# Kernel tuning notes

Hardware: AMD Instinct MI355X
Metric: run time of the kernel (lower is better)

The kernel has to match this reference:

```python
import jax, jax.numpy as jnp
import numpy as np

N_CFG, N_AST, N_PT, N_FT = 20000, 100000, 50, 10
NUM_NODES = {'cfg': N_CFG, 'ast': N_AST, 'pt': N_PT, 'ft': N_FT}
# canonical etypes as (src_type, dst_type); order matches the W/b stacks
ETYPES = [('cfg', 'cfg'), ('ast', 'ast'), ('ast', 'cfg'), ('cfg', 'ast'),
          ('pt', 'cfg'), ('cfg', 'pt'), ('ft', 'cfg'), ('cfg', 'ft')]
E_COUNTS = [80000, 300000, 100000, 100000, 100000, 100000, 40000, 40000]
H = 128
LAB_F, CON_F = 80, 300
NUM_CLASSES = 2


def hetero_gcn_layer(h, W, b, edge_src, edge_dst):
    """Per-etype linear on src feats, copy_u message, per-etype mean reduce,
    'sum' cross-etype reduce (DGL hetero-GCN pattern used by GCNLayerOld)."""
    out = {nt: 0.0 for nt in NUM_NODES}
    for i, (st, dt) in enumerate(ETYPES):
        Wh = h[st] @ W[i] + b[i]                       # [N_src, d_out]
        m = Wh[edge_src[i]]                            # [E, d_out] gather
        s = jax.ops.segment_sum(m, edge_dst[i], num_segments=NUM_NODES[dt])
        cnt = jax.ops.segment_sum(jnp.ones((m.shape[0],), m.dtype),
                                  edge_dst[i], num_segments=NUM_NODES[dt])
        out[dt] = out[dt] + s / jnp.maximum(cnt, 1.0)[:, None]
    return out


def setup_inputs():
    key = jax.random.key(0)
    ks = iter(jax.random.split(key, 64))
    inp = {}
    inp['cfg_label'] = jax.random.uniform(next(ks), (N_CFG, LAB_F), jnp.float32)
    inp['cfg_content'] = jax.random.normal(next(ks), (N_CFG, CON_F), jnp.float32)
    inp['ast_label'] = jax.random.uniform(next(ks), (N_AST, LAB_F), jnp.float32)
    inp['ast_content'] = jax.random.normal(next(ks), (N_AST, CON_F), jnp.float32)
    names = ['cfgcfg', 'astast', 'astcfg', 'cfgast', 'ptcfg', 'cfgpt', 'ftcfg', 'cfgft']
    for nm, (st, dt), ne in zip(names, ETYPES, E_COUNTS):
        inp['src_' + nm] = jax.random.randint(next(ks), (ne,), 0, NUM_NODES[st], jnp.int32)
        inp['dst_' + nm] = jax.random.randint(next(ks), (ne,), 0, NUM_NODES[dt], jnp.int32)

    def lin(k, shape):
        s = 1.0 / np.sqrt(shape[-2])
        return jax.random.uniform(k, shape, jnp.float32, -s, s)

    inp['W_cfg_lab'] = lin(next(ks), (LAB_F, H // 2)); inp['b_cfg_lab'] = 0.01 * jax.random.normal(next(ks), (H // 2,), jnp.float32)
    inp['W_cfg_con'] = lin(next(ks), (CON_F, H // 2)); inp['b_cfg_con'] = 0.01 * jax.random.normal(next(ks), (H // 2,), jnp.float32)
    inp['W_ast_lab'] = lin(next(ks), (LAB_F, H // 2)); inp['b_ast_lab'] = 0.01 * jax.random.normal(next(ks), (H // 2,), jnp.float32)
    inp['W_ast_con'] = lin(next(ks), (CON_F, H // 2)); inp['b_ast_con'] = 0.01 * jax.random.normal(next(ks), (H // 2,), jnp.float32)
    inp['ptest_emb'] = jax.random.normal(next(ks), (H,), jnp.float32)
    inp['ftest_emb'] = jax.random.normal(next(ks), (H,), jnp.float32)
    for nm, (din, dout) in zip(['1', '2', '3', '4', '5'],
                               [(H, H), (H, H), (2 * H, 2 * H), (2 * H, 2 * H), (4 * H, H)]):
        inp['W' + nm] = lin(next(ks), (8, din, dout))
        inp['b' + nm] = 0.01 * jax.random.normal(next(ks), (8, dout), jnp.float32)
    inp['W_dec'] = lin(next(ks), (H, NUM_CLASSES))
    inp['b_dec'] = 0.01 * jax.random.normal(next(ks), (NUM_CLASSES,), jnp.float32)
    return inp


def reference(cfg_label, cfg_content, ast_label, ast_content,
              src_cfgcfg, dst_cfgcfg, src_astast, dst_astast,
              src_astcfg, dst_astcfg, src_cfgast, dst_cfgast,
              src_ptcfg, dst_ptcfg, src_cfgpt, dst_cfgpt,
              src_ftcfg, dst_ftcfg, src_cfgft, dst_cfgft,
              W_cfg_lab, b_cfg_lab, W_cfg_con, b_cfg_con,
              W_ast_lab, b_ast_lab, W_ast_con, b_ast_con,
              ptest_emb, ftest_emb,
              W1, b1, W2, b2, W3, b3, W4, b4, W5, b5, W_dec, b_dec):
    edge_src = [src_cfgcfg, src_astast, src_astcfg, src_cfgast,
                src_ptcfg, src_cfgpt, src_ftcfg, src_cfgft]
    edge_dst = [dst_cfgcfg, dst_astast, dst_astcfg, dst_cfgast,
                dst_ptcfg, dst_cfgpt, dst_ftcfg, dst_cfgft]
    # per-type encoders / embedding broadcast
    h = {
        'cfg': jnp.concatenate([cfg_label @ W_cfg_lab + b_cfg_lab,
                                cfg_content @ W_cfg_con + b_cfg_con], -1),
        'ast': jnp.concatenate([ast_label @ W_ast_lab + b_ast_lab,
                                ast_content @ W_ast_con + b_ast_con], -1),
        'pt': jnp.broadcast_to(ptest_emb, (N_PT, H)),
        'ft': jnp.broadcast_to(ftest_emb, (N_FT, H)),
    }
    h = hetero_gcn_layer(h, W1, b1, edge_src, edge_dst)
    saved = h
    h = hetero_gcn_layer(h, W2, b2, edge_src, edge_dst)
    h = {nt: jnp.concatenate([saved[nt], h[nt]], -1) for nt in h}   # [*, 2H]
    h = hetero_gcn_layer(h, W3, b3, edge_src, edge_dst)
    saved = h
    h = hetero_gcn_layer(h, W4, b4, edge_src, edge_dst)
    h = {nt: jnp.concatenate([saved[nt], h[nt]], -1) for nt in h}   # [*, 4H]
    h = hetero_gcn_layer(h, W5, b5, edge_src, edge_dst)             # [*, H]
    cfg_logits = h['cfg'] @ W_dec + b_dec
    ast_logits = h['ast'] @ W_dec + b_dec
    # [2*(N_CFG+N_AST), num_classes]: cfg logits, cfg pred, ast logits, ast pred
    return jnp.concatenate([cfg_logits, jax.nn.softmax(cfg_logits, -1),
                            ast_logits, jax.nn.softmax(ast_logits, -1)], 0)
```

## Files before the change

kernel.cpp:

```cpp
#include <hip/hip_runtime.h>

#define BM 64
#define BN 64
#define BK 16

__global__ __launch_bounds__(256) void gemm_bias_kernel(
    const float* __restrict__ A, int lda,
    const float* __restrict__ W,
    const float* __restrict__ bias,
    float* __restrict__ C, int ldc, int col0,
    int N, int K, int DOUT)
{
    __shared__ float As[BK][BM + 4];
    __shared__ float Bs[BK][BN + 4];
    const int tid = threadIdx.x;
    const int tx = tid & 15, ty = tid >> 4;
    const int m0 = blockIdx.x * BM, n0 = blockIdx.y * BN;
    float acc[4][4] = {};
    const int ar = tid >> 2, ak = (tid & 3) << 2;
    const int br = tid >> 4, bn = (tid & 15) << 2;

    for (int k0 = 0; k0 < K; k0 += BK) {
        float4 av = make_float4(0.f, 0.f, 0.f, 0.f);
        int grow = m0 + ar, gk = k0 + ak;
        if (grow < N) {
            if (gk + 3 < K) {
                av = *(const float4*)(A + (long long)grow * lda + gk);
            } else {
                float t0 = 0.f, t1 = 0.f, t2 = 0.f, t3 = 0.f;
                if (gk + 0 < K) t0 = A[(long long)grow * lda + gk + 0];
                if (gk + 1 < K) t1 = A[(long long)grow * lda + gk + 1];
                if (gk + 2 < K) t2 = A[(long long)grow * lda + gk + 2];
                if (gk + 3 < K) t3 = A[(long long)grow * lda + gk + 3];
                av = make_float4(t0, t1, t2, t3);
            }
        }
        As[ak + 0][ar] = av.x; As[ak + 1][ar] = av.y;
        As[ak + 2][ar] = av.z; As[ak + 3][ar] = av.w;

        float4 bv = make_float4(0.f, 0.f, 0.f, 0.f);
        int gbk = k0 + br, gn = n0 + bn;
        if (gbk < K && gn + 3 < DOUT)
            bv = *(const float4*)(W + (long long)gbk * DOUT + gn);
        *(float4*)&Bs[br][bn] = bv;
        __syncthreads();

        #pragma unroll
        for (int kk = 0; kk < BK; ++kk) {
            float4 a4 = *(const float4*)&As[kk][ty << 2];
            float4 b4 = *(const float4*)&Bs[kk][tx << 2];
            float a[4] = {a4.x, a4.y, a4.z, a4.w};
            float b[4] = {b4.x, b4.y, b4.z, b4.w};
            #pragma unroll
            for (int i = 0; i < 4; ++i)
                #pragma unroll
                for (int j = 0; j < 4; ++j)
                    acc[i][j] = fmaf(a[i], b[j], acc[i][j]);
        }
        __syncthreads();
    }

    #pragma unroll
    for (int i = 0; i < 4; ++i) {
        int gm = m0 + (ty << 2) + i;
        if (gm >= N) continue;
        #pragma unroll
        for (int j = 0; j < 4; ++j) {
            int gn = n0 + (tx << 2) + j;
            if (gn < DOUT)
                C[(long long)gm * ldc + col0 + gn] = acc[i][j] + bias[gn];
        }
    }
}

#define GM 128
#define GN 128
#define GK 16

__global__ __launch_bounds__(256) void gemm128_kernel(
    const float* __restrict__ A, int lda,
    const float* __restrict__ W,
    const float* __restrict__ bias,
    float* __restrict__ C, int ldc, int col0,
    int N, int K, int DOUT)
{
    __shared__ float As[GK][GM + 4];
    __shared__ float Bs[GK][GN + 4];
    const int tid = threadIdx.x;
    const int tx = tid & 15, ty = tid >> 4;
    const int m0 = blockIdx.x * GM, n0 = blockIdx.y * GN;
    float acc[8][8] = {};

    const int ar = tid >> 1, ak = (tid & 1) << 3;
    const int br = tid >> 4, bn = (tid & 15) << 3;

    for (int k0 = 0; k0 < K; k0 += GK) {
        int grow = m0 + ar, gk = k0 + ak;
        float4 a0 = make_float4(0.f, 0.f, 0.f, 0.f), a1 = a0;
        if (grow < N) {
            a0 = *(const float4*)(A + (long long)grow * lda + gk);
            a1 = *(const float4*)(A + (long long)grow * lda + gk + 4);
        }
        As[ak + 0][ar] = a0.x; As[ak + 1][ar] = a0.y;
        As[ak + 2][ar] = a0.z; As[ak + 3][ar] = a0.w;
        As[ak + 4][ar] = a1.x; As[ak + 5][ar] = a1.y;
        As[ak + 6][ar] = a1.z; As[ak + 7][ar] = a1.w;

        int gbk = k0 + br, gn = n0 + bn;
        float4 b0 = *(const float4*)(W + (long long)gbk * DOUT + gn);
        float4 b1 = *(const float4*)(W + (long long)gbk * DOUT + gn + 4);
        *(float4*)&Bs[br][bn] = b0;
        *(float4*)&Bs[br][bn + 4] = b1;
        __syncthreads();

        #pragma unroll
        for (int kk = 0; kk < GK; ++kk) {
            float4 aa0 = *(const float4*)&As[kk][ty << 2];
            float4 aa1 = *(const float4*)&As[kk][64 + (ty << 2)];
            float4 bb0 = *(const float4*)&Bs[kk][tx << 2];
            float4 bb1 = *(const float4*)&Bs[kk][64 + (tx << 2)];
            float a[8] = {aa0.x, aa0.y, aa0.z, aa0.w, aa1.x, aa1.y, aa1.z, aa1.w};
            float b[8] = {bb0.x, bb0.y, bb0.z, bb0.w, bb1.x, bb1.y, bb1.z, bb1.w};
            #pragma unroll
            for (int i = 0; i < 8; ++i)
                #pragma unroll
                for (int j = 0; j < 8; ++j)
                    acc[i][j] = fmaf(a[i], b[j], acc[i][j]);
        }
        __syncthreads();
    }

    #pragma unroll
    for (int half = 0; half < 2; ++half) {
        #pragma unroll
        for (int i = 0; i < 4; ++i) {
            int gm = m0 + half * 64 + (ty << 2) + i;
            if (gm >= N) continue;
            int ai = half * 4 + i;
            #pragma unroll
            for (int jh = 0; jh < 2; ++jh) {
                int gn = n0 + jh * 64 + (tx << 2);
                float4 r;
                r.x = acc[ai][jh * 4 + 0] + bias[gn + 0];
                r.y = acc[ai][jh * 4 + 1] + bias[gn + 1];
                r.z = acc[ai][jh * 4 + 2] + bias[gn + 2];
                r.w = acc[ai][jh * 4 + 3] + bias[gn + 3];
                *(float4*)(C + (long long)gm * ldc + col0 + gn) = r;
            }
        }
    }
}

template<int DOUT, bool ACC>
__global__ __launch_bounds__(256) void agg_wave_kernel(
    const float* __restrict__ Wh,
    const int* __restrict__ roff, const int* __restrict__ csr,
    float* __restrict__ out, int ldo, int col0, int N)
{
    constexpr int CT = DOUT / 4;
    constexpr int NPB = 256 / CT;
    const int node = blockIdx.x * NPB + threadIdx.x / CT;
    if (node >= N) return;
    const int c = threadIdx.x % CT;
    const int beg = roff[node], end = roff[node + 1];
    float sx = 0.f, sy = 0.f, sz = 0.f, sw = 0.f;
    for (int e = beg; e < end; ++e) {
        const int s = csr[e];
        const float4 v = *(const float4*)(Wh + (long long)s * DOUT + (c << 2));
        sx += v.x; sy += v.y; sz += v.z; sw += v.w;
    }
    const int deg = end - beg;
    const float sc = deg > 0 ? 1.0f / (float)deg : 0.0f;
    float* po = out + (long long)node * ldo + col0 + (c << 2);
    float4 r; r.x = sx * sc; r.y = sy * sc; r.z = sz * sc; r.w = sw * sc;
    if (ACC) {
        const float4 o = *(const float4*)po;
        r.x += o.x; r.y += o.y; r.z += o.z; r.w += o.w;
    }
    *(float4*)po = r;
}

template<int DOUT>
__global__ __launch_bounds__(256) void agg_part_kernel(
    const float* __restrict__ Wh,
    const int* __restrict__ roff, const int* __restrict__ csr,
    float* __restrict__ P, int SEGS)
{
    constexpr int CT = DOUT / 4;
    constexpr int EP = 256 / CT;
    const int node = blockIdx.x / SEGS;
    const int seg  = blockIdx.x % SEGS;
    const int c = threadIdx.x % CT;
    const int g = threadIdx.x / CT;
    const int beg = roff[node], end = roff[node + 1];
    float sx = 0.f, sy = 0.f, sz = 0.f, sw = 0.f;
    for (int e = beg + seg * EP + g; e < end; e += SEGS * EP) {
        const int s = csr[e];
        const float4 v = *(const float4*)(Wh + (long long)s * DOUT + (c << 2));
        sx += v.x; sy += v.y; sz += v.z; sw += v.w;
    }
    __shared__ float4 red[256];
    red[threadIdx.x] = make_float4(sx, sy, sz, sw);
    __syncthreads();
    if (g == 0) {
        #pragma unroll
        for (int k = 1; k < EP; ++k) {
            const float4 v = red[k * CT + c];
            sx += v.x; sy += v.y; sz += v.z; sw += v.w;
        }
        float* pp = P + (long long)node * DOUT + (c << 2);
        atomicAdd(pp + 0, sx);
        atomicAdd(pp + 1, sy);
        atomicAdd(pp + 2, sz);
        atomicAdd(pp + 3, sw);
    }
}

__global__ void agg_fin_kernel(const float* __restrict__ P,
                               const int* __restrict__ roff,
                               float* __restrict__ out, int ldo, int col0,
                               int N, int DOUT)
{
    int idx = blockIdx.x * blockDim.x + threadIdx.x;
    if (idx >= N * DOUT) return;
    int n = idx / DOUT, c = idx % DOUT;
    int deg = roff[n + 1] - roff[n];
    float sc = deg > 0 ? 1.0f / (float)deg : 0.0f;
    out[(long long)n * ldo + col0 + c] = P[idx] * sc;
}

__global__ void zero_f32_kernel(float* __restrict__ p, int n)
{
    int i = blockIdx.x * blockDim.x + threadIdx.x;
    if (i < n) p[i] = 0.f;
}

__global__ void zero_i32_kernel(int* __restrict__ p, int n)
{
    int i = blockIdx.x * blockDim.x + threadIdx.x;
    if (i < n) p[i] = 0;
}

__global__ void count_kernel(const int* __restrict__ dst, int E, int* __restrict__ cnt)
{
    int i = blockIdx.x * blockDim.x + threadIdx.x;
    if (i < E) atomicAdd(&cnt[dst[i]], 1);
}

struct ScanParams { int off[8]; int N[8]; };

__global__ __launch_bounds__(1024) void scan8_kernel(
    const int* __restrict__ cnt_all, int* __restrict__ roff_all, ScanParams p)
{
    const int et = blockIdx.x;
    const int* cnt = cnt_all + p.off[et];
    int* roff = roff_all + p.off[et] + et;
    const int N = p.N[et];
    __shared__ int sh[1024];
    __shared__ int carry_sh;
    if (threadIdx.x == 0) carry_sh = 0;
    __syncthreads();
    for (int base = 0; base < N; base += 1024) {
        const int i = base + threadIdx.x;
        const int v = (i < N) ? cnt[i] : 0;
        sh[threadIdx.x] = v;
        __syncthreads();
        int incl = v;
        for (int ofs = 1; ofs < 1024; ofs <<= 1) {
            const int t = (threadIdx.x >= (unsigned)ofs) ? sh[threadIdx.x - ofs] : 0;
            __syncthreads();
            incl += t;
            sh[threadIdx.x] = incl;
            __syncthreads();
        }
        const int carry = carry_sh;
        if (i < N) roff[i] = carry + incl - v;
        __syncthreads();
        if (threadIdx.x == 1023) carry_sh = carry + incl;
        __syncthreads();
    }
    if (threadIdx.x == 0) roff[N] = carry_sh;
}

__global__ void fill_kernel(const int* __restrict__ src, const int* __restrict__ dst,
                            int E, const int* __restrict__ roff,
                            int* __restrict__ cur, int* __restrict__ csr)
{
    int i = blockIdx.x * blockDim.x + threadIdx.x;
    if (i < E) {
        const int d = dst[i];
        const int pos = atomicAdd(&cur[d], 1);
        csr[roff[d] + pos] = src[i];
    }
}

__global__ void bcast_kernel(const float* __restrict__ emb, float* __restrict__ Fp,
                             int ld, int N)
{
    int idx = blockIdx.x * blockDim.x + threadIdx.x;
    if (idx >= N * 128) return;
    int r = idx >> 7, c = idx & 127;
    Fp[(long long)r * ld + c] = emb[c];
}

__global__ void decoder_kernel(const float* __restrict__ H, int ld, int N,
                               const float* __restrict__ Wd,
                               const float* __restrict__ bd,
                               float* __restrict__ logits, float* __restrict__ soft)
{
    int n = blockIdx.x * blockDim.x + threadIdx.x;
    if (n >= N) return;
    const float* h = H + (long long)n * ld;
    float s0 = bd[0], s1 = bd[1];
    #pragma unroll
    for (int k = 0; k < 128; k += 4) {
        float4 hv = *(const float4*)(h + k);
        s0 = fmaf(hv.x, Wd[2 * (k + 0) + 0], s0); s1 = fmaf(hv.x, Wd[2 * (k + 0) + 1], s1);
        s0 = fmaf(hv.y, Wd[2 * (k + 1) + 0], s0); s1 = fmaf(hv.y, Wd[2 * (k + 1) + 1], s1);
        s0 = fmaf(hv.z, Wd[2 * (k + 2) + 0], s0); s1 = fmaf(hv.z, Wd[2 * (k + 2) + 1], s1);
        s0 = fmaf(hv.w, Wd[2 * (k + 3) + 0], s0); s1 = fmaf(hv.w, Wd[2 * (k + 3) + 1], s1);
    }
    logits[2 * n + 0] = s0;
    logits[2 * n + 1] = s1;
    float m = fmaxf(s0, s1);
    float e0 = expf(s0 - m), e1 = expf(s1 - m);
    float invs = 1.f / (e0 + e1);
    soft[2 * n + 0] = e0 * invs;
    soft[2 * n + 1] = e1 * invs;
}

extern "C" void kernel_launch(void* const* d_in, const int* in_sizes, int n_in,
                              void* d_out, int out_size, void* d_ws, size_t ws_size,
                              hipStream_t stream)
{
    enum { CFG = 0, AST = 1, PT = 2, FT = 3 };
    const int Nnt[4] = {20000, 100000, 50, 10};
    const int stp[8] = {CFG, AST, AST, CFG, PT, CFG, FT, CFG};
    const int dtp[8] = {CFG, AST, CFG, AST, CFG, PT, CFG, FT};
    const bool firstw[8] = {true, true, false, false, false, true, false, true};

    const float* cfg_label   = (const float*)d_in[0];
    const float* cfg_content = (const float*)d_in[1];
    const float* ast_label   = (const float*)d_in[2];
    const float* ast_content = (const float*)d_in[3];
    const int* esrc[8]; const int* edst[8]; int E[8];
    for (int i = 0; i < 8; ++i) {
        esrc[i] = (const int*)d_in[4 + 2 * i];
        edst[i] = (const int*)d_in[5 + 2 * i];
        E[i]    = in_sizes[4 + 2 * i];
    }
    const float* W_cfg_lab = (const float*)d_in[20]; const float* b_cfg_lab = (const float*)d_in[21];
    const float* W_cfg_con = (const float*)d_in[22]; const float* b_cfg_con = (const float*)d_in[23];
    const float* W_ast_lab = (const float*)d_in[24]; const float* b_ast_lab = (const float*)d_in[25];
    const float* W_ast_con = (const float*)d_in[26]; const float* b_ast_con = (const float*)d_in[27];
    const float* ptest_emb = (const float*)d_in[28];
    const float* ftest_emb = (const float*)d_in[29];
    const float* Wl[5] = {(const float*)d_in[30], (const float*)d_in[32], (const float*)d_in[34],
                          (const float*)d_in[36], (const float*)d_in[38]};
    const float* bl[5] = {(const float*)d_in[31], (const float*)d_in[33], (const float*)d_in[35],
                          (const float*)d_in[37], (const float*)d_in[39]};
    const float* W_dec = (const float*)d_in[40];
    const float* b_dec = (const float*)d_in[41];

    char* ws = (char*)d_ws;
    size_t off = 0;
    auto carve = [&](size_t bytes) -> void* {
        void* p = ws + off;
        off = (off + bytes + 255) & ~(size_t)255;
        return p;
    };
    float* F[4];  float* F2[4];
    F[CFG]  = (float*)carve((size_t)20000  * 512 * 4);
    F[AST]  = (float*)carve((size_t)100000 * 512 * 4);
    F[PT]   = (float*)carve((size_t)50     * 512 * 4);
    F[FT]   = (float*)carve((size_t)10     * 512 * 4);
    F2[CFG] = (float*)carve((size_t)20000  * 256 * 4);
    F2[AST] = (float*)carve((size_t)100000 * 256 * 4);
    F2[PT]  = (float*)carve((size_t)50     * 256 * 4);
    F2[FT]  = (float*)carve((size_t)10     * 256 * 4);
    float* Wh = (float*)carve((size_t)100000 * 256 * 4);
    float* P  = (float*)carve((size_t)50 * 256 * 4);

    int Nd[8], cntoff[8], roffoff[8], csroff[8];
    int totc = 0, tote = 0;
    for (int i = 0; i < 8; ++i) {
        Nd[i] = Nnt[dtp[i]];
        cntoff[i] = totc; roffoff[i] = totc + i; csroff[i] = tote;
        totc += Nd[i]; tote += E[i];
    }
    int* cnt_all  = (int*)carve((size_t)totc * 4);
    int* cur_all  = (int*)carve((size_t)totc * 4);
    int* roff_all = (int*)carve((size_t)(totc + 8) * 4);
    int* csr_all  = (int*)carve((size_t)tote * 4);

    zero_i32_kernel<<<(totc + 255) / 256, 256, 0, stream>>>(cnt_all, totc);
    zero_i32_kernel<<<(totc + 255) / 256, 256, 0, stream>>>(cur_all, totc);
    for (int i = 0; i < 8; ++i)
        count_kernel<<<(E[i] + 255) / 256, 256, 0, stream>>>(edst[i], E[i], cnt_all + cntoff[i]);
    ScanParams sp;
    for (int i = 0; i < 8; ++i) { sp.off[i] = cntoff[i]; sp.N[i] = Nd[i]; }
    scan8_kernel<<<8, 1024, 0, stream>>>(cnt_all, roff_all, sp);
    for (int i = 0; i < 8; ++i)
        fill_kernel<<<(E[i] + 255) / 256, 256, 0, stream>>>(
            esrc[i], edst[i], E[i], roff_all + roffoff[i], cur_all + cntoff[i],
            csr_all + csroff[i]);

    {
        dim3 g1((20000 + BM - 1) / BM, 1), g2((100000 + BM - 1) / BM, 1);
        gemm_bias_kernel<<<g1, 256, 0, stream>>>(cfg_label, 80, W_cfg_lab, b_cfg_lab,
                                                 F[CFG], 512, 0, 20000, 80, 64);
        gemm_bias_kernel<<<g1, 256, 0, stream>>>(cfg_content, 300, W_cfg_con, b_cfg_con,
                                                 F[CFG], 512, 64, 20000, 300, 64);
        gemm_bias_kernel<<<g2, 256, 0, stream>>>(ast_label, 80, W_ast_lab, b_ast_lab,
                                                 F[AST], 512, 0, 100000, 80, 64);
        gemm_bias_kernel<<<g2, 256, 0, stream>>>(ast_content, 300, W_ast_con, b_ast_con,
                                                 F[AST], 512, 64, 100000, 300, 64);
    }
    bcast_kernel<<<(50 * 128 + 255) / 256, 256, 0, stream>>>(ptest_emb, F[PT], 512, 50);
    bcast_kernel<<<(10 * 128 + 255) / 256, 256, 0, stream>>>(ftest_emb, F[FT], 512, 10);

    auto launch_agg = [&](int i, int dout, float* outp, int ldo, int col0) {
        const int* roff = roff_all + roffoff[i];
        const int* csr  = csr_all + csroff[i];
        const int Ndst  = Nd[i];
        const bool acc  = !firstw[i];
        if (i == 5 || i == 7) {
            const int SEGS = (Ndst <= 10) ? 204 : 40;
            zero_f32_kernel<<<(Ndst * dout + 255) / 256, 256, 0, stream>>>(P, Ndst * dout);
            if (dout == 128)
                agg_part_kernel<128><<<Ndst * SEGS, 256, 0, stream>>>(Wh, roff, csr, P, SEGS);
            else
                agg_part_kernel<256><<<Ndst * SEGS, 256, 0, stream>>>(Wh, roff, csr, P, SEGS);
            agg_fin_kernel<<<(Ndst * dout + 255) / 256, 256, 0, stream>>>(
                P, roff, outp, ldo, col0, Ndst, dout);
            return;
        }
        if (dout == 128) {
            int grid = (Ndst + 7) / 8;
            if (acc) agg_wave_kernel<128, true ><<<grid, 256, 0, stream>>>(Wh, roff, csr, outp, ldo, col0, Ndst);
            else     agg_wave_kernel<128, false><<<grid, 256, 0, stream>>>(Wh, roff, csr, outp, ldo, col0, Ndst);
        } else {
            int grid = (Ndst + 3) / 4;
            if (acc) agg_wave_kernel<256, true ><<<grid, 256, 0, stream>>>(Wh, roff, csr, outp, ldo, col0, Ndst);
            else     agg_wave_kernel<256, false><<<grid, 256, 0, stream>>>(Wh, roff, csr, outp, ldo, col0, Ndst);
        }
    };

    auto run_layer = [&](const float* Wstack, const float* bstack, int din, int dout,
                         float* const* inB, int ldin, float* const* outB, int ldout,
                         int colout) {
        for (int i = 0; i < 8; ++i) {
            const int s = stp[i], d = dtp[i];
            dim3 g((Nnt[s] + GM - 1) / GM, dout / GN);
            gemm128_kernel<<<g, 256, 0, stream>>>(
                inB[s], ldin, Wstack + (size_t)i * din * dout, bstack + (size_t)i * dout,
                Wh, dout, 0, Nnt[s], din, dout);
            launch_agg(i, dout, outB[d], ldout, colout);
        }
    };

    run_layer(Wl[0], bl[0], 128, 128, F,  512, F2, 256, 0);
    run_layer(Wl[1], bl[1], 128, 128, F2, 256, F2, 256, 128);
    run_layer(Wl[2], bl[2], 256, 256, F2, 256, F,  512, 0);
    run_layer(Wl[3], bl[3], 256, 256, F,  512, F,  512, 256);
    run_layer(Wl[4], bl[4], 512, 128, F,  512, F2, 256, 0);

    float* out = (float*)d_out;
    decoder_kernel<<<(20000 + 255) / 256, 256, 0, stream>>>(
        F2[CFG], 256, 20000, W_dec, b_dec, out + 0, out + 40000);
    decoder_kernel<<<(100000 + 255) / 256, 256, 0, stream>>>(
        F2[AST], 256, 100000, W_dec, b_dec, out + 80000, out + 280000);
}
```

Measured before the change: 4.755 ms.

## Batch cfg-source etype GEMMs, double-buffer GEMM tiles, parallelize CSR scan

Packs the weights of the four cfg-source edge types into one wide matrix, so a single GEMM reads the cfg features once and produces all four transforms. The aggregation kernels then read their slice with a stride and column offset. The 128x128 GEMM now double-buffers its shared-memory tiles, prefetching the next K slice into registers while the current one is computed, which halves the barriers per step. The single-block-per-etype CSR scan becomes a three-phase multi-block scan, and the tiny pt/ft source GEMMs move to the 64-tile kernel. The trade-offs are an extra weight-packing kernel per layer, a larger Wh buffer, and strided gathers in aggregation.

Result: slower. 4.875 ms (+2.5%).

```diff
diff --git a/kernel.cpp b/kernel.cpp
--- a/kernel.cpp
+++ b/kernel.cpp
@@ -84,8 +84,8 @@
     float* __restrict__ C, int ldc, int col0,
     int N, int K, int DOUT)
 {
-    __shared__ float As[GK][GM + 4];
-    __shared__ float Bs[GK][GN + 4];
+    __shared__ float As[2][GK][GM + 4];
+    __shared__ float Bs[2][GK][GN + 4];
     const int tid = threadIdx.x;
     const int tx = tid & 15, ty = tid >> 4;
     const int m0 = blockIdx.x * GM, n0 = blockIdx.y * GN;
@@ -93,32 +93,44 @@
 
     const int ar = tid >> 1, ak = (tid & 1) << 3;
     const int br = tid >> 4, bn = (tid & 15) << 3;
-
-    for (int k0 = 0; k0 < K; k0 += GK) {
-        int grow = m0 + ar, gk = k0 + ak;
-        float4 a0 = make_float4(0.f, 0.f, 0.f, 0.f), a1 = a0;
-        if (grow < N) {
-            a0 = *(const float4*)(A + (long long)grow * lda + gk);
-            a1 = *(const float4*)(A + (long long)grow * lda + gk + 4);
-        }
-        As[ak + 0][ar] = a0.x; As[ak + 1][ar] = a0.y;
-        As[ak + 2][ar] = a0.z; As[ak + 3][ar] = a0.w;
-        As[ak + 4][ar] = a1.x; As[ak + 5][ar] = a1.y;
-        As[ak + 6][ar] = a1.z; As[ak + 7][ar] = a1.w;
-
-        int gbk = k0 + br, gn = n0 + bn;
-        float4 b0 = *(const float4*)(W + (long long)gbk * DOUT + gn);
-        float4 b1 = *(const float4*)(W + (long long)gbk * DOUT + gn + 4);
-        *(float4*)&Bs[br][bn] = b0;
-        *(float4*)&Bs[br][bn + 4] = b1;
+    const long long arow = (long long)(m0 + ar) * lda;
+    const bool aval = (m0 + ar) < N;
+
+    float4 pa0 = make_float4(0.f,0.f,0.f,0.f), pa1 = pa0, pb0, pb1;
+    if (aval) {
+        pa0 = *(const float4*)(A + arow + ak);
+        pa1 = *(const float4*)(A + arow + ak + 4);
+    }
+    pb0 = *(const float4*)(W + (long long)br * DOUT + n0 + bn);
+    pb1 = *(const float4*)(W + (long long)br * DOUT + n0 + bn + 4);
+
+    As[0][ak + 0][ar] = pa0.x; As[0][ak + 1][ar] = pa0.y;
+    As[0][ak + 2][ar] = pa0.z; As[0][ak + 3][ar] = pa0.w;
+    As[0][ak + 4][ar] = pa1.x; As[0][ak + 5][ar] = pa1.y;
+    As[0][ak + 6][ar] = pa1.z; As[0][ak + 7][ar] = pa1.w;
+    *(float4*)&Bs[0][br][bn]     = pb0;
+    *(float4*)&Bs[0][br][bn + 4] = pb1;
+
+    const int nt = K / GK;
+    int cur = 0;
+    for (int t = 0; t < nt; ++t) {
         __syncthreads();
-
+        if (t + 1 < nt) {
+            const int gk = (t + 1) * GK;
+            pa0 = make_float4(0.f,0.f,0.f,0.f); pa1 = pa0;
+            if (aval) {
+                pa0 = *(const float4*)(A + arow + gk + ak);
+                pa1 = *(const float4*)(A + arow + gk + ak + 4);
+            }
+            pb0 = *(const float4*)(W + (long long)(gk + br) * DOUT + n0 + bn);
+            pb1 = *(const float4*)(W + (long long)(gk + br) * DOUT + n0 + bn + 4);
+        }
         #pragma unroll
         for (int kk = 0; kk < GK; ++kk) {
-            float4 aa0 = *(const float4*)&As[kk][ty << 2];
-            float4 aa1 = *(const float4*)&As[kk][64 + (ty << 2)];
-            float4 bb0 = *(const float4*)&Bs[kk][tx << 2];
-            float4 bb1 = *(const float4*)&Bs[kk][64 + (tx << 2)];
+            float4 aa0 = *(const float4*)&As[cur][kk][ty << 2];
+            float4 aa1 = *(const float4*)&As[cur][kk][64 + (ty << 2)];
+            float4 bb0 = *(const float4*)&Bs[cur][kk][tx << 2];
+            float4 bb1 = *(const float4*)&Bs[cur][kk][64 + (tx << 2)];
             float a[8] = {aa0.x, aa0.y, aa0.z, aa0.w, aa1.x, aa1.y, aa1.z, aa1.w};
             float b[8] = {bb0.x, bb0.y, bb0.z, bb0.w, bb1.x, bb1.y, bb1.z, bb1.w};
             #pragma unroll
@@ -127,7 +139,16 @@
                 for (int j = 0; j < 8; ++j)
                     acc[i][j] = fmaf(a[i], b[j], acc[i][j]);
         }
-        __syncthreads();
+        if (t + 1 < nt) {
+            const int nb = cur ^ 1;
+            As[nb][ak + 0][ar] = pa0.x; As[nb][ak + 1][ar] = pa0.y;
+            As[nb][ak + 2][ar] = pa0.z; As[nb][ak + 3][ar] = pa0.w;
+            As[nb][ak + 4][ar] = pa1.x; As[nb][ak + 5][ar] = pa1.y;
+            As[nb][ak + 6][ar] = pa1.z; As[nb][ak + 7][ar] = pa1.w;
+            *(float4*)&Bs[nb][br][bn]     = pb0;
+            *(float4*)&Bs[nb][br][bn + 4] = pb1;
+        }
+        cur ^= 1;
     }
 
     #pragma unroll
@@ -151,9 +172,29 @@
     }
 }
 
+__global__ void pack_w_kernel(const float* __restrict__ Wstack,
+                              const float* __restrict__ bstack,
+                              int din, int dout, int4 etl,
+                              float* __restrict__ Bp, float* __restrict__ bp)
+{
+    const int idx = blockIdx.x * blockDim.x + threadIdx.x;
+    const int wtot = din * 4 * dout;
+    if (idx < wtot) {
+        const int col = idx % (4 * dout), k = idx / (4 * dout);
+        const int et = col / dout, c = col % dout;
+        const int e = (&etl.x)[et];
+        Bp[idx] = Wstack[((size_t)e * din + k) * dout + c];
+    }
+    if (idx < 4 * dout) {
+        const int et = idx / dout, c = idx % dout;
+        const int e = (&etl.x)[et];
+        bp[idx] = bstack[e * dout + c];
+    }
+}
+
 template<int DOUT, bool ACC>
 __global__ __launch_bounds__(256) void agg_wave_kernel(
-    const float* __restrict__ Wh,
+    const float* __restrict__ Wh, int ldWh, int colWh,
     const int* __restrict__ roff, const int* __restrict__ csr,
     float* __restrict__ out, int ldo, int col0, int N)
 {
@@ -166,7 +207,7 @@
     float sx = 0.f, sy = 0.f, sz = 0.f, sw = 0.f;
     for (int e = beg; e < end; ++e) {
         const int s = csr[e];
-        const float4 v = *(const float4*)(Wh + (long long)s * DOUT + (c << 2));
+        const float4 v = *(const float4*)(Wh + (long long)s * ldWh + colWh + (c << 2));
         sx += v.x; sy += v.y; sz += v.z; sw += v.w;
     }
     const int deg = end - beg;
@@ -182,7 +223,7 @@
 
 template<int DOUT>
 __global__ __launch_bounds__(256) void agg_part_kernel(
-    const float* __restrict__ Wh,
+    const float* __restrict__ Wh, int ldWh, int colWh,
     const int* __restrict__ roff, const int* __restrict__ csr,
     float* __restrict__ P, int SEGS)
 {
@@ -196,7 +237,7 @@
     float sx = 0.f, sy = 0.f, sz = 0.f, sw = 0.f;
     for (int e = beg + seg * EP + g; e < end; e += SEGS * EP) {
         const int s = csr[e];
-        const float4 v = *(const float4*)(Wh + (long long)s * DOUT + (c << 2));
+        const float4 v = *(const float4*)(Wh + (long long)s * ldWh + colWh + (c << 2));
         sx += v.x; sy += v.y; sz += v.z; sw += v.w;
     }
     __shared__ float4 red[256];
@@ -247,50 +288,67 @@
     if (i < E) atomicAdd(&cnt[dst[i]], 1);
 }
 
-struct ScanParams { int off[8]; int N[8]; };
-
-__global__ __launch_bounds__(1024) void scan8_kernel(
-    const int* __restrict__ cnt_all, int* __restrict__ roff_all, ScanParams p)
-{
-    const int et = blockIdx.x;
-    const int* cnt = cnt_all + p.off[et];
-    int* roff = roff_all + p.off[et] + et;
-    const int N = p.N[et];
-    __shared__ int sh[1024];
-    __shared__ int carry_sh;
-    if (threadIdx.x == 0) carry_sh = 0;
+#define SCB 256
+#define SCI 4
+__global__ __launch_bounds__(SCB) void scan_p1_kernel(
+    const int* __restrict__ cnt, int n, int* __restrict__ G, int* __restrict__ bsum)
+{
+    __shared__ int sh[SCB];
+    const int base = blockIdx.x * (SCB * SCI);
+    const int tb = base + threadIdx.x * SCI;
+    int v[SCI]; int tsum = 0;
+    #pragma unroll
+    for (int j = 0; j < SCI; ++j) {
+        int idx = tb + j;
+        v[j] = (idx < n) ? cnt[idx] : 0;
+        tsum += v[j];
+    }
+    sh[threadIdx.x] = tsum;
     __syncthreads();
-    for (int base = 0; base < N; base += 1024) {
-        const int i = base + threadIdx.x;
-        const int v = (i < N) ? cnt[i] : 0;
-        sh[threadIdx.x] = v;
+    int incl = tsum;
+    for (int ofs = 1; ofs < SCB; ofs <<= 1) {
+        int t = (threadIdx.x >= (unsigned)ofs) ? sh[threadIdx.x - ofs] : 0;
         __syncthreads();
-        int incl = v;
-        for (int ofs = 1; ofs < 1024; ofs <<= 1) {
-            const int t = (threadIdx.x >= (unsigned)ofs) ? sh[threadIdx.x - ofs] : 0;
-            __syncthreads();
-            incl += t;
-            sh[threadIdx.x] = incl;
-            __syncthreads();
-        }
-        const int carry = carry_sh;
-        if (i < N) roff[i] = carry + incl - v;
+        incl += t;
+        sh[threadIdx.x] = incl;
         __syncthreads();
-        if (threadIdx.x == 1023) carry_sh = carry + incl;
-        __syncthreads();
-    }
-    if (threadIdx.x == 0) roff[N] = carry_sh;
+    }
+    if (threadIdx.x == SCB - 1) bsum[blockIdx.x] = incl;
+    int run = incl - tsum;
+    #pragma unroll
+    for (int j = 0; j < SCI; ++j) {
+        int idx = tb + j;
+        if (idx < n) G[idx] = run;
+        run += v[j];
+    }
+}
+
+__global__ void scan_p2_kernel(int* __restrict__ bsum, int nb)
+{
+    if (blockIdx.x == 0 && threadIdx.x == 0) {
+        int run = 0;
+        for (int b = 0; b < nb; ++b) { int t = bsum[b]; bsum[b] = run; run += t; }
+    }
+}
+
+__global__ void scan_p3_kernel(int* __restrict__ G, int n,
+                               const int* __restrict__ bsum, int tote)
+{
+    int i = blockIdx.x * blockDim.x + threadIdx.x;
+    if (i < n) G[i] += bsum[i / (SCB * SCI)];
+    if (i == 0) G[n] = tote;
 }
 
 __global__ void fill_kernel(const int* __restrict__ src, const int* __restrict__ dst,
-                            int E, const int* __restrict__ roff,
-                            int* __restrict__ cur, int* __restrict__ csr)
+                            int E, const int* __restrict__ G,
+                            int* __restrict__ cur,
+                            int* __restrict__ csr)
 {
     int i = blockIdx.x * blockDim.x + threadIdx.x;
     if (i < E) {
         const int d = dst[i];
         const int pos = atomicAdd(&cur[d], 1);
-        csr[roff[d] + pos] = src[i];
+        csr[G[d] + pos] = src[i];
     }
 }
 
@@ -335,9 +393,7 @@
 {
     enum { CFG = 0, AST = 1, PT = 2, FT = 3 };
     const int Nnt[4] = {20000, 100000, 50, 10};
-    const int stp[8] = {CFG, AST, AST, CFG, PT, CFG, FT, CFG};
     const int dtp[8] = {CFG, AST, CFG, AST, CFG, PT, CFG, FT};
-    const bool firstw[8] = {true, true, false, false, false, true, false, true};
 
     const float* cfg_label   = (const float*)d_in[0];
     const float* cfg_content = (const float*)d_in[1];
@@ -378,32 +434,39 @@
     F2[AST] = (float*)carve((size_t)100000 * 256 * 4);
     F2[PT]  = (float*)carve((size_t)50     * 256 * 4);
     F2[FT]  = (float*)carve((size_t)10     * 256 * 4);
-    float* Wh = (float*)carve((size_t)100000 * 256 * 4);
-    float* P  = (float*)carve((size_t)50 * 256 * 4);
-
-    int Nd[8], cntoff[8], roffoff[8], csroff[8];
+    float* WhS = (float*)carve((size_t)100000 * 256 * 4);
+    float* WhA = WhS;
+    float* WhC = WhS;
+    float* WhP = (float*)carve((size_t)50  * 256 * 4);
+    float* WhF = (float*)carve((size_t)10  * 256 * 4);
+    float* P   = (float*)carve((size_t)50  * 256 * 4);
+    float* Bp  = (float*)carve((size_t)512 * 1024 * 4);
+    float* bp  = (float*)carve((size_t)1024 * 4);
+
+    int Nd[8], cntoff[8];
     int totc = 0, tote = 0;
     for (int i = 0; i < 8; ++i) {
         Nd[i] = Nnt[dtp[i]];
-        cntoff[i] = totc; roffoff[i] = totc + i; csroff[i] = tote;
+        cntoff[i] = totc;
         totc += Nd[i]; tote += E[i];
     }
-    int* cnt_all  = (int*)carve((size_t)totc * 4);
-    int* cur_all  = (int*)carve((size_t)totc * 4);
-    int* roff_all = (int*)carve((size_t)(totc + 8) * 4);
-    int* csr_all  = (int*)carve((size_t)tote * 4);
+    int* cnt_all = (int*)carve((size_t)totc * 4);
+    int* cur_all = (int*)carve((size_t)totc * 4);
+    int* G       = (int*)carve((size_t)(totc + 1) * 4);
+    const int nb = (totc + SCB * SCI - 1) / (SCB * SCI);
+    int* bsum    = (int*)carve((size_t)nb * 4);
+    int* csr_all = (int*)carve((size_t)tote * 4);
 
     zero_i32_kernel<<<(totc + 255) / 256, 256, 0, stream>>>(cnt_all, totc);
     zero_i32_kernel<<<(totc + 255) / 256, 256, 0, stream>>>(cur_all, totc);
     for (int i = 0; i < 8; ++i)
         count_kernel<<<(E[i] + 255) / 256, 256, 0, stream>>>(edst[i], E[i], cnt_all + cntoff[i]);
-    ScanParams sp;
-    for (int i = 0; i < 8; ++i) { sp.off[i] = cntoff[i]; sp.N[i] = Nd[i]; }
-    scan8_kernel<<<8, 1024, 0, stream>>>(cnt_all, roff_all, sp);
+    scan_p1_kernel<<<nb, SCB, 0, stream>>>(cnt_all, totc, G, bsum);
+    scan_p2_kernel<<<1, 64, 0, stream>>>(bsum, nb);
+    scan_p3_kernel<<<(totc + 255) / 256, 256, 0, stream>>>(G, totc, bsum, tote);
     for (int i = 0; i < 8; ++i)
         fill_kernel<<<(E[i] + 255) / 256, 256, 0, stream>>>(
-            esrc[i], edst[i], E[i], roff_all + roffoff[i], cur_all + cntoff[i],
-            csr_all + csroff[i]);
+            esrc[i], edst[i], E[i], G + cntoff[i], cur_all + cntoff[i], csr_all);
 
     {
         dim3 g1((20000 + BM - 1) / BM, 1), g2((100000 + BM - 1) / BM, 1);
@@ -419,43 +482,77 @@
     bcast_kernel<<<(50 * 128 + 255) / 256, 256, 0, stream>>>(ptest_emb, F[PT], 512, 50);
     bcast_kernel<<<(10 * 128 + 255) / 256, 256, 0, stream>>>(ftest_emb, F[FT], 512, 10);
 
-    auto launch_agg = [&](int i, int dout, float* outp, int ldo, int col0) {
-        const int* roff = roff_all + roffoff[i];
-        const int* csr  = csr_all + csroff[i];
+    auto agg = [&](int i, int dout, const float* Whp, int ldWh, int colWh,
+                   float* outp, int ldo, int col0, bool acc) {
+        const int* roff = G + cntoff[i];
         const int Ndst  = Nd[i];
-        const bool acc  = !firstw[i];
-        if (i == 5 || i == 7) {
-            const int SEGS = (Ndst <= 10) ? 204 : 40;
-            zero_f32_kernel<<<(Ndst * dout + 255) / 256, 256, 0, stream>>>(P, Ndst * dout);
-            if (dout == 128)
-                agg_part_kernel<128><<<Ndst * SEGS, 256, 0, stream>>>(Wh, roff, csr, P, SEGS);
-            else
-                agg_part_kernel<256><<<Ndst * SEGS, 256, 0, stream>>>(Wh, roff, csr, P, SEGS);
-            agg_fin_kernel<<<(Ndst * dout + 255) / 256, 256, 0, stream>>>(
-                P, roff, outp, ldo, col0, Ndst, dout);
-            return;
-        }
         if (dout == 128) {
             int grid = (Ndst + 7) / 8;
-            if (acc) agg_wave_kernel<128, true ><<<grid, 256, 0, stream>>>(Wh, roff, csr, outp, ldo, col0, Ndst);
-            else     agg_wave_kernel<128, false><<<grid, 256, 0, stream>>>(Wh, roff, csr, outp, ldo, col0, Ndst);
+            if (acc) agg_wave_kernel<128, true ><<<grid, 256, 0, stream>>>(Whp, ldWh, colWh, roff, csr_all, outp, ldo, col0, Ndst);
+            else     agg_wave_kernel<128, false><<<grid, 256, 0, stream>>>(Whp, ldWh, colWh, roff, csr_all, outp, ldo, col0, Ndst);
         } else {
             int grid = (Ndst + 3) / 4;
-            if (acc) agg_wave_kernel<256, true ><<<grid, 256, 0, stream>>>(Wh, roff, csr, outp, ldo, col0, Ndst);
-            else     agg_wave_kernel<256, false><<<grid, 256, 0, stream>>>(Wh, roff, csr, outp, ldo, col0, Ndst);
-        }
+            if (acc) agg_wave_kernel<256, true ><<<grid, 256, 0, stream>>>(Whp, ldWh, colWh, roff, csr_all, outp, ldo, col0, Ndst);
+            else     agg_wave_kernel<256, false><<<grid, 256, 0, stream>>>(Whp, ldWh, colWh, roff, csr_all, outp, ldo, col0, Ndst);
+        }
+    };
+    auto aggP = [&](int i, int dout, const float* Whp, int ldWh, int colWh,
+                    float* outp, int ldo, int col0) {
+        const int* roff = G + cntoff[i];
+        const int Ndst  = Nd[i];
+        const int SEGS  = (Ndst <= 10) ? 204 : 40;
+        zero_f32_kernel<<<(Ndst * dout + 255) / 256, 256, 0, stream>>>(P, Ndst * dout);
+        if (dout == 128)
+            agg_part_kernel<128><<<Ndst * SEGS, 256, 0, stream>>>(Whp, ldWh, colWh, roff, csr_all, P, SEGS);
+        else
+            agg_part_kernel<256><<<Ndst * SEGS, 256, 0, stream>>>(Whp, ldWh, colWh, roff, csr_all, P, SEGS);
+        agg_fin_kernel<<<(Ndst * dout + 255) / 256, 256, 0, stream>>>(
+            P, roff, outp, ldo, col0, Ndst, dout);
     };
 
     auto run_layer = [&](const float* Wstack, const float* bstack, int din, int dout,
                          float* const* inB, int ldin, float* const* outB, int ldout,
                          int colout) {
-        for (int i = 0; i < 8; ++i) {
-            const int s = stp[i], d = dtp[i];
-            dim3 g((Nnt[s] + GM - 1) / GM, dout / GN);
+        const int wtot = din * 4 * dout;
+        pack_w_kernel<<<(wtot + 255) / 256, 256, 0, stream>>>(
+            Wstack, bstack, din, dout, make_int4(0, 3, 5, 7), Bp, bp);
+
+        {
+            dim3 g((100000 + GM - 1) / GM, dout / GN);
             gemm128_kernel<<<g, 256, 0, stream>>>(
-                inB[s], ldin, Wstack + (size_t)i * din * dout, bstack + (size_t)i * dout,
-                Wh, dout, 0, Nnt[s], din, dout);
-            launch_agg(i, dout, outB[d], ldout, colout);
+                inB[AST], ldin, Wstack + (size_t)1 * din * dout, bstack + 1 * dout,
+                WhA, dout, 0, 100000, din, dout);
+            agg(1, dout, WhA, dout, 0, outB[AST], ldout, colout, false);
+        }
+        {
+            dim3 g((100000 + GM - 1) / GM, dout / GN);
+            gemm128_kernel<<<g, 256, 0, stream>>>(
+                inB[AST], ldin, Wstack + (size_t)2 * din * dout, bstack + 2 * dout,
+                WhA, dout, 0, 100000, din, dout);
+            agg(2, dout, WhA, dout, 0, outB[CFG], ldout, colout, false);
+        }
+        {
+            dim3 g((20000 + GM - 1) / GM, (4 * dout) / GN);
+            gemm128_kernel<<<g, 256, 0, stream>>>(
+                inB[CFG], ldin, Bp, bp, WhC, 4 * dout, 0, 20000, din, 4 * dout);
+            agg (0, dout, WhC, 4 * dout, 0 * dout, outB[CFG], ldout, colout, true);
+            agg (3, dout, WhC, 4 * dout, 1 * dout, outB[AST], ldout, colout, true);
+            aggP(5, dout, WhC, 4 * dout, 2 * dout, outB[PT],  ldout, colout);
+            aggP(7, dout, WhC, 4 * dout, 3 * dout, outB[FT],  ldout, colout);
+        }
+        {
+            dim3 g(1, dout / BN);
+            gemm_bias_kernel<<<g, 256, 0, stream>>>(
+                inB[PT], ldin, Wstack + (size_t)4 * din * dout, bstack + 4 * dout,
+                WhP, dout, 0, 50, din, dout);
+            agg(4, dout, WhP, dout, 0, outB[CFG], ldout, colout, true);
+        }
+        {
+            dim3 g(1, dout / BN);
+            gemm_bias_kernel<<<g, 256, 0, stream>>>(
+                inB[FT], ldin, Wstack + (size_t)6 * din * dout, bstack + 6 * dout,
+                WhF, dout, 0, 10, din, dout);
+            agg(6, dout, WhF, dout, 0, outB[CFG], ldout, colout, true);
         }
     };
 
```
